# Kernel optimization log

Hardware: AMD Instinct MI355X
Metric: run time of the kernel (lower is better)

Reference implementation:

```python
import jax, jax.numpy as jnp
import numpy as np

N, E, H, D, FE = 50000, 400000, 4, 64, 64  # nodes, edges, heads, per-head dim, edge feat dim
NEG_SLOPE = 0.2


def setup_inputs() -> dict:
    key = jax.random.key(0)
    ks = jax.random.split(key, 18)
    def p(k, shape, s=0.1):
        return jax.random.normal(k, shape, dtype=jnp.float32) * s
    return dict(
        features=p(ks[0], (N, D), 1.0),
        edge_feat=p(ks[1], (E, FE), 1.0),
        src=jax.random.randint(ks[2], (E,), 0, N),
        dst=jax.random.randint(ks[3], (E,), 0, N),
        # layer 0: in=64 -> H*D=256, residual Linear since 64 != 256
        W0=p(ks[4], (D, H * D)), We0=p(ks[5], (FE, H * D)),
        al0=p(ks[6], (H, D)), ar0=p(ks[7], (H, D)), ae0=p(ks[8], (H, D)),
        b0=p(ks[9], (H * D,)), Wres0=p(ks[10], (D, H * D)),
        # layer 1 (last): in=256 -> H*D=256, residual = identity view
        W1=p(ks[11], (H * D, H * D)), We1=p(ks[12], (FE, H * D)),
        al1=p(ks[13], (H, D)), ar1=p(ks[14], (H, D)), ae1=p(ks[15], (H, D)),
        b1=p(ks[16], (H * D,)),
    )


def _edge_gat_layer(h, ef, src, dst, W, We, al, ar, ae, b, Wres=None):
    n = h.shape[0]
    ft = (h @ W).reshape(n, H, D)          # (N,H,D) projected node feats
    fe = (ef @ We).reshape(-1, H, D)       # (E,H,D) projected edge feats
    el = jnp.sum(ft * al, axis=-1)         # (N,H)
    er = jnp.sum(ft * ar, axis=-1)         # (N,H)
    ee = jnp.sum(fe * ae, axis=-1)         # (E,H)
    e = el[src] + er[dst] + ee             # (E,H)
    e = jnp.where(e > 0, e, NEG_SLOPE * e)  # leaky_relu(0.2)
    # segment softmax over incoming edges of each dst node
    m = jax.ops.segment_max(jax.lax.stop_gradient(e), dst, num_segments=n)
    ex = jnp.exp(e - m[dst])
    den = jax.ops.segment_sum(ex, dst, num_segments=n)
    a = ex / den[dst]                      # (E,H) attention
    out = jax.ops.segment_sum(ft[src] * a[:, :, None], dst, num_segments=n)  # (N,H,D)
    res = (h @ Wres).reshape(n, H, D) if Wres is not None else h.reshape(n, H, D)
    return out + res + b.reshape(1, H, D)


def reference(features, edge_feat, src, dst,
              W0, We0, al0, ar0, ae0, b0, Wres0,
              W1, We1, al1, ar1, ae1, b1):
    h = _edge_gat_layer(features, edge_feat, src, dst, W0, We0, al0, ar0, ae0, b0, Wres0)
    h = jax.nn.elu(h.reshape(N, H * D))    # flatten heads + ELU between layers
    h = _edge_gat_layer(h, edge_feat, src, dst, W1, We1, al1, ar1, ae1, b1)
    return h.mean(axis=1)                  # (N, D) mean over heads on last layer
```

## Files before the change

### kernel.cpp

```cpp
#include <hip/hip_runtime.h>
#include <hip/hip_bf16.h>

#define NN 50000
#define EE 400000
#define NB 196

typedef __bf16 bf16_8 __attribute__((ext_vector_type(8)));
typedef float f32x4 __attribute__((ext_vector_type(4)));

__global__ __launch_bounds__(256) void prep_kernel(
    const float* __restrict__ features, __bf16* __restrict__ fbf,
    const float* __restrict__ W0, const float* __restrict__ Wres0, __bf16* __restrict__ Bt0,
    const float* __restrict__ W1, __bf16* __restrict__ Bt1,
    const float* __restrict__ We0, const float* __restrict__ ae0, float* __restrict__ Ve0,
    const float* __restrict__ We1, const float* __restrict__ ae1, float* __restrict__ Ve1,
    const int* __restrict__ dst, int* __restrict__ cnt) {
  int b = blockIdx.x;
  int t = threadIdx.x;
  if (b < 1563) {
    int i = b * 256 + t;
    if (i < NN * 64 / 8) {
      const float4* p = (const float4*)features + (size_t)i * 2;
      float4 a = p[0], c = p[1];
      bf16_8 v = {(__bf16)a.x, (__bf16)a.y, (__bf16)a.z, (__bf16)a.w,
                  (__bf16)c.x, (__bf16)c.y, (__bf16)c.z, (__bf16)c.w};
      *(bf16_8*)(fbf + (size_t)i * 8) = v;
    }
  } else if (b < 1563 + 128) {
    int idx = (b - 1563) * 256 + t;
    int j = idx >> 6, k = idx & 63;
    float v = (j < 256) ? W0[k * 256 + j] : Wres0[k * 256 + (j - 256)];
    Bt0[idx] = (__bf16)v;
  } else if (b < 1563 + 128 + 256) {
    int idx = (b - 1563 - 128) * 256 + t;
    int j = idx >> 8, k = idx & 255;
    Bt1[idx] = (__bf16)W1[k * 256 + j];
  } else if (b == 1947) {
    int f = t >> 2, h = t & 3;
    float s = 0.f;
    for (int d = 0; d < 64; ++d) s += We0[f * 256 + h * 64 + d] * ae0[h * 64 + d];
    Ve0[f * 4 + h] = s;
  } else if (b == 1948) {
    int f = t >> 2, h = t & 3;
    float s = 0.f;
    for (int d = 0; d < 64; ++d) s += We1[f * 256 + h * 64 + d] * ae1[h * 64 + d];
    Ve1[f * 4 + h] = s;
  } else {
    int e = (b - 1949) * 256 + t;
    if (e < EE) atomicAdd(&cnt[dst[e]], 1);
  }
}

__global__ __launch_bounds__(256) void scan1_kernel(const int* __restrict__ cnt,
                                                    int* __restrict__ scanbuf,
                                                    int* __restrict__ blocksum) {
  __shared__ int s[256];
  int t = threadIdx.x;
  int idx = blockIdx.x * 256 + t;
  int c = (idx < NN) ? cnt[idx] : 0;
  s[t] = c;
  __syncthreads();
  for (int d = 1; d < 256; d <<= 1) {
    int v = (t >= d) ? s[t - d] : 0;
    __syncthreads();
    s[t] += v;
    __syncthreads();
  }
  if (idx < NN) scanbuf[idx] = s[t];
  if (t == 255) blocksum[blockIdx.x] = s[255];
}

__global__ __launch_bounds__(256) void scan2_kernel(const int* __restrict__ blocksum,
                                                    int* __restrict__ blockoff, int nb) {
  __shared__ int s[256];
  int t = threadIdx.x;
  int c = (t < nb) ? blocksum[t] : 0;
  s[t] = c;
  __syncthreads();
  for (int d = 1; d < 256; d <<= 1) {
    int v = (t >= d) ? s[t - d] : 0;
    __syncthreads();
    s[t] += v;
    __syncthreads();
  }
  if (t < nb) blockoff[t] = s[t] - c;
}

__global__ __launch_bounds__(256) void scan3_kernel(const int* __restrict__ scanbuf,
                                                    const int* __restrict__ cnt,
                                                    const int* __restrict__ blockoff,
                                                    int* __restrict__ off,
                                                    int* __restrict__ cur) {
  int idx = blockIdx.x * 256 + threadIdx.x;
  if (idx < NN) {
    int o = blockoff[blockIdx.x] + scanbuf[idx] - cnt[idx];
    off[idx] = o;
    cur[idx] = o;
  }
  if (idx == 0) off[NN] = EE;
}

__global__ __launch_bounds__(256) void fill_kernel(const int* __restrict__ src,
                                                   const int* __restrict__ dst,
                                                   int* __restrict__ cur,
                                                   int* __restrict__ srcc,
                                                   int* __restrict__ pose) {
  int e = blockIdx.x * 256 + threadIdx.x;
  if (e < EE) {
    int p = atomicAdd(&cur[dst[e]], 1);
    srcc[p] = src[e];
    pose[e] = p;
  }
}

__global__ __launch_bounds__(256) void eek_kernel(const float* __restrict__ ef,
                                                  const float* __restrict__ Ve0,
                                                  const float* __restrict__ Ve1,
                                                  float* __restrict__ eeo0,
                                                  float* __restrict__ eeo1) {
  __shared__ float V0[256], V1[256];
  V0[threadIdx.x] = Ve0[threadIdx.x];
  V1[threadIdx.x] = Ve1[threadIdx.x];
  __syncthreads();
  int r = threadIdx.x >> 2, sub = threadIdx.x & 3;
  int e = blockIdx.x * 64 + r;
  if (e >= EE) return;
  float a0 = 0, a1 = 0, a2 = 0, a3 = 0;
  float c0 = 0, c1 = 0, c2 = 0, c3 = 0;
  const float* row = ef + (size_t)e * 64 + sub * 16;
#pragma unroll
  for (int i = 0; i < 16; i += 4) {
    float4 v = *(const float4*)(row + i);
    float xs[4] = {v.x, v.y, v.z, v.w};
#pragma unroll
    for (int j = 0; j < 4; ++j) {
      float x = xs[j];
      int idx = (sub * 16 + i + j) * 4;
      a0 += x * V0[idx + 0]; a1 += x * V0[idx + 1];
      a2 += x * V0[idx + 2]; a3 += x * V0[idx + 3];
      c0 += x * V1[idx + 0]; c1 += x * V1[idx + 1];
      c2 += x * V1[idx + 2]; c3 += x * V1[idx + 3];
    }
  }
#pragma unroll
  for (int o = 1; o < 4; o <<= 1) {
    a0 += __shfl_xor(a0, o); a1 += __shfl_xor(a1, o);
    a2 += __shfl_xor(a2, o); a3 += __shfl_xor(a3, o);
    c0 += __shfl_xor(c0, o); c1 += __shfl_xor(c1, o);
    c2 += __shfl_xor(c2, o); c3 += __shfl_xor(c3, o);
  }
  if (sub == 0) {
    float4 u; u.x = a0; u.y = a1; u.z = a2; u.w = a3;
    float4 w; w.x = c0; w.y = c1; w.z = c2; w.w = c3;
    *(float4*)(eeo0 + (size_t)e * 4) = u;
    *(float4*)(eeo1 + (size_t)e * 4) = w;
  }
}

#define LDK 40
__global__ __launch_bounds__(256) void gemm_kernel(const __bf16* __restrict__ A,
                                                   const __bf16* __restrict__ Bt,
                                                   __bf16* __restrict__ ft,
                                                   __bf16* __restrict__ base,
                                                   const float* __restrict__ bias,
                                                   const float* __restrict__ al,
                                                   const float* __restrict__ ar,
                                                   float* __restrict__ el,
                                                   float* __restrict__ er,
                                                   int M, int K) {
  __shared__ __align__(16) __bf16 Al[64 * LDK];
  __shared__ __align__(16) __bf16 Bl[64 * LDK];
  int tid = threadIdx.x;
  int wav = tid >> 6, lane = tid & 63;
  int quad = lane >> 4, l16 = lane & 15;
  int bm = blockIdx.x * 64;
  int bn = blockIdx.y * 64;
  int sr = tid >> 2;
  int sk = (tid & 3) << 3;

  f32x4 acc[4] = {{0, 0, 0, 0}, {0, 0, 0, 0}, {0, 0, 0, 0}, {0, 0, 0, 0}};

  for (int k0 = 0; k0 < K; k0 += 32) {
    uint4 av = {0, 0, 0, 0};
    int arow = bm + sr;
    if (arow < M) av = *(const uint4*)(A + (size_t)arow * K + k0 + sk);
    uint4 bv = *(const uint4*)(Bt + (size_t)(bn + sr) * K + k0 + sk);
    __syncthreads();
    *(uint4*)&Al[sr * LDK + sk] = av;
    *(uint4*)&Bl[sr * LDK + sk] = bv;
    __syncthreads();
    bf16_8 af = *(const bf16_8*)&Al[(wav * 16 + l16) * LDK + quad * 8];
#pragma unroll
    for (int nt = 0; nt < 4; ++nt) {
      bf16_8 bf = *(const bf16_8*)&Bl[(nt * 16 + l16) * LDK + quad * 8];
      acc[nt] = __builtin_amdgcn_mfma_f32_16x16x32_bf16(af, bf, acc[nt], 0, 0, 0);
    }
  }

  int row0 = bm + wav * 16 + quad * 4;

  if (bn < 256) {
    int hb = bn >> 6;
#pragma unroll
    for (int r = 0; r < 4; ++r) {
      float pl = 0.f, pr = 0.f;
#pragma unroll
      for (int nt = 0; nt < 4; ++nt) {
        float v = acc[nt][r];
        int d = nt * 16 + l16;
        pl += v * al[hb * 64 + d];
        pr += v * ar[hb * 64 + d];
      }
#pragma unroll
      for (int o2 = 8; o2 > 0; o2 >>= 1) {
        pl += __shfl_xor(pl, o2);
        pr += __shfl_xor(pr, o2);
      }
      int row = row0 + r;
      if (l16 == 0 && row < M) {
        el[row * 4 + hb] = pl;
        er[row * 4 + hb] = pr;
      }
    }
  }

#pragma unroll
  for (int nt = 0; nt < 4; ++nt) {
    int col = bn + nt * 16 + l16;
#pragma unroll
    for (int r = 0; r < 4; ++r) {
      int row = row0 + r;
      if (row < M) {
        float v = acc[nt][r];
        if (col < 256)
          ft[(size_t)row * 256 + col] = (__bf16)v;
        else
          base[(size_t)row * 256 + (col - 256)] = (__bf16)(v + bias[col - 256]);
      }
    }
  }
}

__global__ __launch_bounds__(256) void wk_kernel(const int* __restrict__ src,
                                                 const int* __restrict__ dst,
                                                 const int* __restrict__ pose,
                                                 const float* __restrict__ ee,
                                                 const float* __restrict__ el,
                                                 const float* __restrict__ er,
                                                 float* __restrict__ wcsr) {
  int e = blockIdx.x * 256 + threadIdx.x;
  if (e >= EE) return;
  int s = src[e], d = dst[e], p = pose[e];
  float4 z4 = *(const float4*)(ee + (size_t)e * 4);
  float4 e_l = *(const float4*)(el + (size_t)s * 4);
  float4 e_r = *(const float4*)(er + (size_t)d * 4);
  float4 w;
  float z;
  z = e_l.x + e_r.x + z4.x; w.x = __expf(z > 0.f ? z : 0.2f * z);
  z = e_l.y + e_r.y + z4.y; w.y = __expf(z > 0.f ? z : 0.2f * z);
  z = e_l.z + e_r.z + z4.z; w.z = __expf(z > 0.f ? z : 0.2f * z);
  z = e_l.w + e_r.w + z4.w; w.w = __expf(z > 0.f ? z : 0.2f * z);
  *(float4*)(wcsr + (size_t)p * 4) = w;
}

template <int LAYER>
__global__ __launch_bounds__(256) void agg_kernel(const int* __restrict__ off,
                                                  const int* __restrict__ srcc,
                                                  const float* __restrict__ wcsr,
                                                  const __bf16* __restrict__ ft,
                                                  const __bf16* prev,
                                                  const float* __restrict__ bias,
                                                  __bf16* outb,
                                                  float* __restrict__ outf) {
  __shared__ float red[256];
  int n = blockIdx.x;
  int t = threadIdx.x, h = t >> 6, lane = t & 63;
  int beg = off[n], end = off[n + 1];
  float pv = (float)prev[(size_t)n * 256 + t];
  float bv = (LAYER == 1) ? bias[t] : 0.f;
  int offd = h * 64 + lane;

  float acc = 0.f, den = 0.f;
  for (int c = beg; c < end; c += 64) {
    int rem = end - c;
    if (rem > 64) rem = 64;
    int sv = 0;
    float wv = 0.f;
    if (lane < rem) {
      sv = srcc[c + lane];
      wv = wcsr[(size_t)(c + lane) * 4 + h];
    }
    int k = 0;
    for (; k + 4 <= rem; k += 4) {
      int s0 = __builtin_amdgcn_readlane(sv, k);
      int s1 = __builtin_amdgcn_readlane(sv, k + 1);
      int s2 = __builtin_amdgcn_readlane(sv, k + 2);
      int s3 = __builtin_amdgcn_readlane(sv, k + 3);
      float w0 = __uint_as_float(__builtin_amdgcn_readlane(__float_as_uint(wv), k));
      float w1 = __uint_as_float(__builtin_amdgcn_readlane(__float_as_uint(wv), k + 1));
      float w2 = __uint_as_float(__builtin_amdgcn_readlane(__float_as_uint(wv), k + 2));
      float w3 = __uint_as_float(__builtin_amdgcn_readlane(__float_as_uint(wv), k + 3));
      float v0 = (float)ft[(size_t)s0 * 256 + offd];
      float v1 = (float)ft[(size_t)s1 * 256 + offd];
      float v2 = (float)ft[(size_t)s2 * 256 + offd];
      float v3 = (float)ft[(size_t)s3 * 256 + offd];
      acc += w0 * v0; acc += w1 * v1; acc += w2 * v2; acc += w3 * v3;
      den += w0 + w1 + w2 + w3;
    }
    for (; k < rem; ++k) {
      int s = __builtin_amdgcn_readlane(sv, k);
      float w = __uint_as_float(__builtin_amdgcn_readlane(__float_as_uint(wv), k));
      acc += w * (float)ft[(size_t)s * 256 + offd];
      den += w;
    }
  }
  float res = (end > beg) ? acc / den : 0.f;

  if (LAYER == 0) {
    float v = res + pv;
    v = v > 0.f ? v : (__expf(v) - 1.0f);
    outb[(size_t)n * 256 + t] = (__bf16)v;
  } else {
    red[t] = res + pv + bv;
    __syncthreads();
    if (t < 64)
      outf[(size_t)n * 64 + t] =
          0.25f * (red[t] + red[t + 64] + red[t + 128] + red[t + 192]);
  }
}

extern "C" void kernel_launch(void* const* d_in, const int* in_sizes, int n_in,
                              void* d_out, int out_size, void* d_ws, size_t ws_size,
                              hipStream_t stream) {
  const float* features  = (const float*)d_in[0];
  const float* edge_feat = (const float*)d_in[1];
  const int*   src       = (const int*)d_in[2];
  const int*   dst       = (const int*)d_in[3];
  const float* W0    = (const float*)d_in[4];
  const float* We0   = (const float*)d_in[5];
  const float* al0   = (const float*)d_in[6];
  const float* ar0   = (const float*)d_in[7];
  const float* ae0   = (const float*)d_in[8];
  const float* b0    = (const float*)d_in[9];
  const float* Wres0 = (const float*)d_in[10];
  const float* W1    = (const float*)d_in[11];
  const float* We1   = (const float*)d_in[12];
  const float* al1   = (const float*)d_in[13];
  const float* ar1   = (const float*)d_in[14];
  const float* ae1   = (const float*)d_in[15];
  const float* b1    = (const float*)d_in[16];
  float* out = (float*)d_out;

  char* ws = (char*)d_ws;
  size_t o = 0;
  auto alloc = [&](size_t bytes) {
    void* p = ws + o;
    o = (o + bytes + 255) & ~(size_t)255;
    return p;
  };
  int*    cnt      = (int*)alloc((size_t)NN * 4);
  int*    scanbuf  = (int*)alloc((size_t)NN * 4);
  int*    blocksum = (int*)alloc(256 * 4);
  int*    blockoff = (int*)alloc(256 * 4);
  int*    off      = (int*)alloc((size_t)(NN + 1) * 4);
  int*    cur      = (int*)alloc((size_t)NN * 4);
  int*    srcc     = (int*)alloc((size_t)EE * 4);
  int*    pose     = (int*)alloc((size_t)EE * 4);
  float*  eeo0     = (float*)alloc((size_t)EE * 4 * 4);
  float*  eeo1     = (float*)alloc((size_t)EE * 4 * 4);
  float*  wcsr     = (float*)alloc((size_t)EE * 4 * 4);
  float*  el       = (float*)alloc((size_t)NN * 4 * 4);
  float*  er       = (float*)alloc((size_t)NN * 4 * 4);
  float*  Ve0      = (float*)alloc(256 * 4);
  float*  Ve1      = (float*)alloc(256 * 4);
  __bf16* Bt0      = (__bf16*)alloc((size_t)512 * 64 * 2);
  __bf16* Bt1      = (__bf16*)alloc((size_t)256 * 256 * 2);
  __bf16* fbf      = (__bf16*)alloc((size_t)NN * 64 * 2);
  __bf16* ft       = (__bf16*)alloc((size_t)NN * 256 * 2);
  __bf16* base     = (__bf16*)alloc((size_t)NN * 256 * 2);
  __bf16* h1       = base;

  const int EB = (EE + 255) / 256;
  const int MG = (NN + 63) / 64;

  hipMemsetAsync(cnt, 0, (size_t)NN * 4, stream);
  prep_kernel<<<1949 + EB, 256, 0, stream>>>(features, fbf, W0, Wres0, Bt0, W1, Bt1,
                                             We0, ae0, Ve0, We1, ae1, Ve1, dst, cnt);
  scan1_kernel<<<NB, 256, 0, stream>>>(cnt, scanbuf, blocksum);
  scan2_kernel<<<1, 256, 0, stream>>>(blocksum, blockoff, NB);
  scan3_kernel<<<NB, 256, 0, stream>>>(scanbuf, cnt, blockoff, off, cur);
  fill_kernel<<<EB, 256, 0, stream>>>(src, dst, cur, srcc, pose);
  eek_kernel<<<(EE + 63) / 64, 256, 0, stream>>>(edge_feat, Ve0, Ve1, eeo0, eeo1);

  gemm_kernel<<<dim3(MG, 8), 256, 0, stream>>>(fbf, Bt0, ft, base, b0, al0, ar0, el, er, NN, 64);
  wk_kernel<<<EB, 256, 0, stream>>>(src, dst, pose, eeo0, el, er, wcsr);
  agg_kernel<0><<<NN, 256, 0, stream>>>(off, srcc, wcsr, ft, base, nullptr, h1, nullptr);

  gemm_kernel<<<dim3(MG, 4), 256, 0, stream>>>(h1, Bt1, ft, nullptr, nullptr, al1, ar1, el, er, NN, 256);
  wk_kernel<<<EB, 256, 0, stream>>>(src, dst, pose, eeo1, el, er, wcsr);
  agg_kernel<1><<<NN, 256, 0, stream>>>(off, srcc, wcsr, ft, h1, b1, nullptr, out);
}
```

Measured before the change: 436.5 us.

## Process two nodes per block in aggregation with half-wave heads and packed bf16 pairs

The aggregation kernel now handles two destination nodes per 256-thread block. Each half-wave owns one head, and each lane loads two packed bf16 features as one 32-bit word and accumulates them with paired FMAs. Attention weights are staged in shared memory instead of being broadcast with readlane, and the denominator comes from a lane sum plus a shuffle reduction rather than being accumulated per edge. This halves the block count and widens the per-lane loads, at the cost of 32-edge chunks and a shared-memory round trip for the weights.

After: 410.2 us. 1.06x faster.

```diff
diff --git a/kernel.cpp b/kernel.cpp
--- a/kernel.cpp
+++ b/kernel.cpp
@@ -6,7 +6,16 @@
 #define NB 196
 
 typedef __bf16 bf16_8 __attribute__((ext_vector_type(8)));
+typedef __bf16 bf16_2 __attribute__((ext_vector_type(2)));
 typedef float f32x4 __attribute__((ext_vector_type(4)));
+typedef float f32x2 __attribute__((ext_vector_type(2)));
+
+__device__ inline f32x2 bf2(unsigned u) {
+  f32x2 r;
+  r.x = __uint_as_float(u << 16);
+  r.y = __uint_as_float(u & 0xffff0000u);
+  return r;
+}
 
 __global__ __launch_bounds__(256) void prep_kernel(
     const float* __restrict__ features, __bf16* __restrict__ fbf,
@@ -272,60 +281,93 @@
                                                   const float* __restrict__ bias,
                                                   __bf16* outb,
                                                   float* __restrict__ outf) {
-  __shared__ float red[256];
-  int n = blockIdx.x;
-  int t = threadIdx.x, h = t >> 6, lane = t & 63;
+  __shared__ f32x2 wl2[2][4][32];
+  __shared__ f32x2 red2[2][4][32];
+  int t = threadIdx.x;
+  int wav = t >> 6, lane = t & 63;
+  int nh = wav >> 1;
+  int hf = lane >> 5;
+  int head = ((wav & 1) << 1) + hf;
+  int k32 = lane & 31;
+  int n = blockIdx.x * 2 + nh;
   int beg = off[n], end = off[n + 1];
-  float pv = (float)prev[(size_t)n * 256 + t];
-  float bv = (LAYER == 1) ? bias[t] : 0.f;
-  int offd = h * 64 + lane;
-
-  float acc = 0.f, den = 0.f;
-  for (int c = beg; c < end; c += 64) {
+  int offb = head * 128 + k32 * 4;
+
+  const char* ftb = (const char*)ft;
+  f32x2 acc0 = {0.f, 0.f}, acc1 = {0.f, 0.f};
+  float denp = 0.f;
+
+  for (int c = beg; c < end; c += 32) {
     int rem = end - c;
-    if (rem > 64) rem = 64;
+    if (rem > 32) rem = 32;
     int sv = 0;
     float wv = 0.f;
-    if (lane < rem) {
-      sv = srcc[c + lane];
-      wv = wcsr[(size_t)(c + lane) * 4 + h];
-    }
-    int k = 0;
-    for (; k + 4 <= rem; k += 4) {
-      int s0 = __builtin_amdgcn_readlane(sv, k);
-      int s1 = __builtin_amdgcn_readlane(sv, k + 1);
-      int s2 = __builtin_amdgcn_readlane(sv, k + 2);
-      int s3 = __builtin_amdgcn_readlane(sv, k + 3);
-      float w0 = __uint_as_float(__builtin_amdgcn_readlane(__float_as_uint(wv), k));
-      float w1 = __uint_as_float(__builtin_amdgcn_readlane(__float_as_uint(wv), k + 1));
-      float w2 = __uint_as_float(__builtin_amdgcn_readlane(__float_as_uint(wv), k + 2));
-      float w3 = __uint_as_float(__builtin_amdgcn_readlane(__float_as_uint(wv), k + 3));
-      float v0 = (float)ft[(size_t)s0 * 256 + offd];
-      float v1 = (float)ft[(size_t)s1 * 256 + offd];
-      float v2 = (float)ft[(size_t)s2 * 256 + offd];
-      float v3 = (float)ft[(size_t)s3 * 256 + offd];
-      acc += w0 * v0; acc += w1 * v1; acc += w2 * v2; acc += w3 * v3;
-      den += w0 + w1 + w2 + w3;
-    }
-    for (; k < rem; ++k) {
-      int s = __builtin_amdgcn_readlane(sv, k);
-      float w = __uint_as_float(__builtin_amdgcn_readlane(__float_as_uint(wv), k));
-      acc += w * (float)ft[(size_t)s * 256 + offd];
-      den += w;
-    }
-  }
-  float res = (end > beg) ? acc / den : 0.f;
+    if (k32 < rem) {
+      sv = srcc[c + k32];
+      wv = wcsr[(size_t)(c + k32) * 4 + head];
+    }
+    denp += wv;
+    f32x2 wd = {wv, wv};
+    wl2[nh][head][k32] = wd;
+    int kk = 0;
+    for (; kk + 4 <= rem; kk += 4) {
+      int s0 = __builtin_amdgcn_readlane(sv, kk);
+      int s1 = __builtin_amdgcn_readlane(sv, kk + 1);
+      int s2 = __builtin_amdgcn_readlane(sv, kk + 2);
+      int s3 = __builtin_amdgcn_readlane(sv, kk + 3);
+      unsigned u0 = *(const unsigned*)(ftb + (size_t)s0 * 512 + offb);
+      unsigned u1 = *(const unsigned*)(ftb + (size_t)s1 * 512 + offb);
+      unsigned u2 = *(const unsigned*)(ftb + (size_t)s2 * 512 + offb);
+      unsigned u3 = *(const unsigned*)(ftb + (size_t)s3 * 512 + offb);
+      f32x2 w0 = wl2[nh][head][kk];
+      f32x2 w1 = wl2[nh][head][kk + 1];
+      f32x2 w2 = wl2[nh][head][kk + 2];
+      f32x2 w3 = wl2[nh][head][kk + 3];
+      acc0 = __builtin_elementwise_fma(bf2(u0), w0, acc0);
+      acc1 = __builtin_elementwise_fma(bf2(u1), w1, acc1);
+      acc0 = __builtin_elementwise_fma(bf2(u2), w2, acc0);
+      acc1 = __builtin_elementwise_fma(bf2(u3), w3, acc1);
+    }
+    for (; kk < rem; ++kk) {
+      int s0 = __builtin_amdgcn_readlane(sv, kk);
+      unsigned u0 = *(const unsigned*)(ftb + (size_t)s0 * 512 + offb);
+      f32x2 w0 = wl2[nh][head][kk];
+      acc0 = __builtin_elementwise_fma(bf2(u0), w0, acc0);
+    }
+  }
+#pragma unroll
+  for (int m = 16; m; m >>= 1) denp += __shfl_xor(denp, m);
+
+  f32x2 res = {0.f, 0.f};
+  if (end > beg) {
+    float rd = 1.f / denp;
+    res.x = (acc0.x + acc1.x) * rd;
+    res.y = (acc0.y + acc1.y) * rd;
+  }
+
+  unsigned pu = *(const unsigned*)((const char*)prev + (size_t)n * 512 + offb);
+  f32x2 pv = bf2(pu);
 
   if (LAYER == 0) {
-    float v = res + pv;
-    v = v > 0.f ? v : (__expf(v) - 1.0f);
-    outb[(size_t)n * 256 + t] = (__bf16)v;
+    float vx = res.x + pv.x;
+    float vy = res.y + pv.y;
+    vx = vx > 0.f ? vx : (__expf(vx) - 1.0f);
+    vy = vy > 0.f ? vy : (__expf(vy) - 1.0f);
+    bf16_2 o = {(__bf16)vx, (__bf16)vy};
+    *(bf16_2*)((char*)outb + (size_t)n * 512 + offb) = o;
   } else {
-    red[t] = res + pv + bv;
-    __syncthreads();
-    if (t < 64)
-      outf[(size_t)n * 64 + t] =
-          0.25f * (red[t] + red[t + 64] + red[t + 128] + red[t + 192]);
+    f32x2 bv = *(const f32x2*)(bias + head * 64 + 2 * k32);
+    f32x2 rv = {res.x + pv.x + bv.x, res.y + pv.y + bv.y};
+    red2[nh][head][k32] = rv;
+    __syncthreads();
+    if ((wav & 1) == 0 && hf == 0) {
+      f32x2 a = red2[nh][0][k32];
+      f32x2 b = red2[nh][1][k32];
+      f32x2 c = red2[nh][2][k32];
+      f32x2 d = red2[nh][3][k32];
+      f32x2 s = {0.25f * (a.x + b.x + c.x + d.x), 0.25f * (a.y + b.y + c.y + d.y)};
+      *(f32x2*)(outf + (size_t)n * 64 + 2 * k32) = s;
+    }
   }
 }
 
@@ -394,9 +436,9 @@
 
   gemm_kernel<<<dim3(MG, 8), 256, 0, stream>>>(fbf, Bt0, ft, base, b0, al0, ar0, el, er, NN, 64);
   wk_kernel<<<EB, 256, 0, stream>>>(src, dst, pose, eeo0, el, er, wcsr);
-  agg_kernel<0><<<NN, 256, 0, stream>>>(off, srcc, wcsr, ft, base, nullptr, h1, nullptr);
+  agg_kernel<0><<<NN / 2, 256, 0, stream>>>(off, srcc, wcsr, ft, base, nullptr, h1, nullptr);
 
   gemm_kernel<<<dim3(MG, 4), 256, 0, stream>>>(h1, Bt1, ft, nullptr, nullptr, al1, ar1, el, er, NN, 256);
   wk_kernel<<<EB, 256, 0, stream>>>(src, dst, pose, eeo1, el, er, wcsr);
-  agg_kernel<1><<<NN, 256, 0, stream>>>(off, srcc, wcsr, ft, h1, b1, nullptr, out);
-}
+  agg_kernel<1><<<NN / 2, 256, 0, stream>>>(off, srcc, wcsr, ft, h1, b1, nullptr, out);
+}
```
